# Kernel optimization log

Measured on AMD Instinct MI355X. Metric: run time of the kernel, lower is better.

Reference implementation:

```python
import jax, jax.numpy as jnp
import numpy as np

N, IN_DIM, HID, STEPS = 1024, 16, 64, 3
EDGE_P = 0.02


def setup_inputs() -> dict:
    key = jax.random.key(0)
    ks = jax.random.split(key, 10)
    s = 0.1
    A = (jax.random.uniform(ks[0], (N, N)) < EDGE_P).astype(jnp.float32)
    E = jax.random.uniform(ks[1], (N, N), dtype=jnp.float32)
    X = jax.random.normal(ks[2], (N, IN_DIM), dtype=jnp.float32)
    W_enc = jax.random.normal(ks[3], (HID, IN_DIM), dtype=jnp.float32) * s
    b_enc = jnp.zeros((HID,), jnp.float32)
    W_msg = jax.random.normal(ks[4], (HID, HID + 1), dtype=jnp.float32) * s
    b_msg = jnp.zeros((HID,), jnp.float32)
    W_ih = jax.random.normal(ks[5], (3 * HID, HID), dtype=jnp.float32) * s
    W_hh = jax.random.normal(ks[6], (3 * HID, HID), dtype=jnp.float32) * s
    b_ih = jnp.zeros((3 * HID,), jnp.float32)
    b_hh = jnp.zeros((3 * HID,), jnp.float32)
    W_r1 = jax.random.normal(ks[7], (HID, 2 * HID), dtype=jnp.float32) * s
    b_r1 = jnp.zeros((HID,), jnp.float32)
    W_r2 = jax.random.normal(ks[8], (1, HID), dtype=jnp.float32) * s
    b_r2 = jnp.zeros((1,), jnp.float32)
    return dict(A=A, E=E, X=X, W_enc=W_enc, b_enc=b_enc, W_msg=W_msg, b_msg=b_msg,
                W_ih=W_ih, W_hh=W_hh, b_ih=b_ih, b_hh=b_hh,
                W_r1=W_r1, b_r1=b_r1, W_r2=W_r2, b_r2=b_r2,
                source=3, target=7, steps=STEPS)


def _gru_cell(x, h, W_ih, W_hh, b_ih, b_hh):
    # torch.nn.GRUCell semantics, gate order (r, z, n)
    gi = x @ W_ih.T + b_ih
    gh = h @ W_hh.T + b_hh
    ir, iz, inn = jnp.split(gi, 3, axis=-1)
    hr, hz, hn = jnp.split(gh, 3, axis=-1)
    r = jax.nn.sigmoid(ir + hr)
    z = jax.nn.sigmoid(iz + hz)
    nct = jnp.tanh(inn + r * hn)
    return (1.0 - z) * nct + z * h


def reference(A, E, X, W_enc, b_enc, W_msg, b_msg, W_ih, W_hh, b_ih, b_hh,
              W_r1, b_r1, W_r2, b_r2, source, target, steps):
    mask = (A > 0).astype(X.dtype)            # [n, n] neighbor mask (row u -> cols v)
    deg = mask.sum(axis=1, keepdims=True)     # [n, 1]
    Wm_h, w_e = W_msg[:, :-1], W_msg[:, -1]   # split msg Linear: hidden part + edge-scalar column
    h = jnp.tanh(X @ W_enc.T + b_enc)         # [n, hid]

    def step(h, _):
        proj = h @ Wm_h.T + b_msg                              # [n, hid] per-neighbor part
        m = jnp.tanh(proj[None, :, :] + E[:, :, None] * w_e)   # [n, n, hid] message u<-v
        s = jnp.einsum('uv,uvh->uh', mask, m)                  # masked sum over neighbors
        msgs = jnp.where(deg > 0, s / jnp.maximum(deg, 1.0), 0.0)  # mean; zero if no neighbors
        return _gru_cell(msgs, h, W_ih, W_hh, b_ih, b_hh), None

    h, _ = jax.lax.scan(step, h, None, length=steps)
    cat = jnp.concatenate([h[source], h[target]])              # [2*hid]
    hid = jax.nn.relu(cat @ W_r1.T + b_r1)
    out = hid @ W_r2.T + b_r2                                  # [1]
    return jax.nn.sigmoid(out)
```

## Files before the change

kernel.cpp:

```cpp
#include <hip/hip_runtime.h>
#include <math.h>

#define N 1024
#define IN_DIM 16
#define HID 64
#define MAXD 64

__device__ __forceinline__ float sigmoidf_(float x) {
    return 1.0f / (1.0f + __expf(-x));
}
__device__ __forceinline__ float ftanh_(float x) {
    float e = __expf(2.0f * x);
    return 1.0f - 2.0f / (e + 1.0f);
}
__device__ __forceinline__ unsigned rne16_(float f) {
    unsigned u = __float_as_uint(f);
    return (u + 0x7FFFu + ((u >> 16) & 1u)) >> 16;
}
__device__ __forceinline__ float blo_(unsigned u) {
    return __uint_as_float(u << 16);
}
__device__ __forceinline__ float bhi_(unsigned u) {
    return __uint_as_float(u & 0xFFFF0000u);
}

#define WIH_W 6144
#define WHH_W 6144
#define WMSG_W 2048
#define WPACK_W (WIH_W + WHH_W + WMSG_W)

__global__ void init_kernel(const float* __restrict__ X,
                            const float* __restrict__ W_enc,
                            const float* __restrict__ b_enc,
                            const float* __restrict__ W_msg,
                            const float* __restrict__ b_msg,
                            const float* __restrict__ W_ih,
                            const float* __restrict__ W_hh,
                            const float* __restrict__ W_r1,
                            const float* __restrict__ A,
                            const float* __restrict__ E,
                            float* __restrict__ h,
                            float* __restrict__ proj,
                            int* __restrict__ nbr,
                            float* __restrict__ ev,
                            float* __restrict__ deg,
                            unsigned* __restrict__ Wpack,
                            float* __restrict__ Wr1T) {
    int bid = blockIdx.x;
    int tid = threadIdx.x;
    int wave = tid >> 6;
    int lane = tid & 63;

    if (bid < 256) {
        int u = bid * 4 + wave;
        __shared__ float sh[4][HID];
        float acc = b_enc[lane];
#pragma unroll
        for (int k = 0; k < IN_DIM; ++k)
            acc += X[u * IN_DIM + k] * W_enc[lane * IN_DIM + k];
        float hv = tanhf(acc);
        h[u * HID + lane] = hv;
        sh[wave][lane] = hv;
        __syncthreads();
        float pacc = b_msg[lane];
        const float4* h4 = (const float4*)sh[wave];
#pragma unroll
        for (int k4 = 0; k4 < HID / 4; ++k4) {
            float4 hh = h4[k4];
            const float* w = &W_msg[lane * (HID + 1) + k4 * 4];
            pacc += hh.x * w[0] + hh.y * w[1] + hh.z * w[2] + hh.w * w[3];
        }
        proj[u * HID + lane] = pacc;
    } else if (bid < 1280) {
        int u = bid - 256;
        __shared__ unsigned long long balls[16];
        __shared__ int base[16];
        float evr[4];
        bool has[4];
#pragma unroll
        for (int ci = 0; ci < 4; ++ci) {
            int chunk = wave * 4 + ci;
            int v = chunk * 64 + lane;
            float a = A[u * N + v];
            bool hs = (a > 0.0f);
            has[ci] = hs;
            evr[ci] = E[u * N + v];
            unsigned long long b = __ballot(hs);
            if (lane == 0) balls[chunk] = b;
        }
        __syncthreads();
        if (tid == 0) {
            int s = 0;
#pragma unroll
            for (int c = 0; c < 16; ++c) {
                base[c] = s;
                s += __popcll(balls[c]);
            }
            deg[u] = (float)s;
        }
        __syncthreads();
#pragma unroll
        for (int ci = 0; ci < 4; ++ci) {
            int chunk = wave * 4 + ci;
            if (has[ci]) {
                unsigned long long b = balls[chunk];
                int slot = base[chunk] + __popcll(b & ((1ull << lane) - 1ull));
                if (slot < MAXD) {
                    nbr[u * MAXD + slot] = chunk * 64 + lane;
                    ev[u * MAXD + slot] = evr[ci];
                }
            }
        }
    } else {
        int t = (bid - 1280) * 256 + tid;
        if (t < WIH_W) {
            int k2 = t / 192, row = t % 192;
            int k = 2 * k2;
            unsigned lo = rne16_(W_ih[row * 64 + k]);
            unsigned hi = rne16_(W_ih[row * 64 + k + 1]);
            Wpack[t] = lo | (hi << 16);
        } else if (t < WIH_W + WHH_W) {
            int t0 = t - WIH_W;
            int k2 = t0 / 192, row = t0 % 192;
            int k = 2 * k2;
            unsigned lo = rne16_(W_hh[row * 64 + k]);
            unsigned hi = rne16_(W_hh[row * 64 + k + 1]);
            Wpack[t] = lo | (hi << 16);
        } else if (t < WPACK_W) {
            int t0 = t - WIH_W - WHH_W;
            int k2 = t0 >> 6, j = t0 & 63;
            int k = 2 * k2;
            unsigned lo = rne16_(W_msg[j * (HID + 1) + k]);
            unsigned hi = rne16_(W_msg[j * (HID + 1) + k + 1]);
            Wpack[t] = lo | (hi << 16);
        } else if (t < WPACK_W + 8192) {
            int t0 = t - WPACK_W;
            int j = t0 >> 7, k = t0 & 127;
            Wr1T[k * 64 + j] = W_r1[t0];
        }
    }
}

__global__ void step_kernel(const float* __restrict__ proj,
                            const float* __restrict__ W_msg,
                            const float* __restrict__ b_msg,
                            const float* __restrict__ hin,
                            const int* __restrict__ nbr,
                            const float* __restrict__ ev,
                            const float* __restrict__ deg,
                            const unsigned* __restrict__ Wpack,
                            const float* __restrict__ b_ih,
                            const float* __restrict__ b_hh,
                            float* __restrict__ hout,
                            float* __restrict__ projout,
                            int do_proj) {
    int tid = threadIdx.x;
    int wave = tid >> 6;
    int lane = tid & 63;
    int u = blockIdx.x * 4 + wave;

    __shared__ unsigned sw[WPACK_W];
    __shared__ float sm[4][2][HID];

    {
        const uint4* gsrc = (const uint4*)Wpack;
        uint4* dst = (uint4*)sw;
#pragma unroll
        for (int c = 0; c < WPACK_W / 4 / 256; ++c)
            dst[c * 256 + tid] = gsrc[c * 256 + tid];
    }

    float we = W_msg[lane * (HID + 1) + HID];
    float d = deg[u];
    int dn = (int)d;
    float hu = hin[u * HID + lane];
    float sum = 0.0f;
    int i = 0;
    for (; i + 8 <= dn; i += 8) {
        int4 na = *(const int4*)&nbr[u * MAXD + i];
        int4 nb = *(const int4*)&nbr[u * MAXD + i + 4];
        float4 ea = *(const float4*)&ev[u * MAXD + i];
        float4 eb = *(const float4*)&ev[u * MAXD + i + 4];
        float q0 = proj[na.x * HID + lane];
        float q1 = proj[na.y * HID + lane];
        float q2 = proj[na.z * HID + lane];
        float q3 = proj[na.w * HID + lane];
        float q4 = proj[nb.x * HID + lane];
        float q5 = proj[nb.y * HID + lane];
        float q6 = proj[nb.z * HID + lane];
        float q7 = proj[nb.w * HID + lane];
        sum += ftanh_(q0 + ea.x * we) + ftanh_(q1 + ea.y * we)
             + ftanh_(q2 + ea.z * we) + ftanh_(q3 + ea.w * we);
        sum += ftanh_(q4 + eb.x * we) + ftanh_(q5 + eb.y * we)
             + ftanh_(q6 + eb.z * we) + ftanh_(q7 + eb.w * we);
    }
    for (; i + 4 <= dn; i += 4) {
        int4 nb = *(const int4*)&nbr[u * MAXD + i];
        float4 e4 = *(const float4*)&ev[u * MAXD + i];
        float q0 = proj[nb.x * HID + lane];
        float q1 = proj[nb.y * HID + lane];
        float q2 = proj[nb.z * HID + lane];
        float q3 = proj[nb.w * HID + lane];
        sum += ftanh_(q0 + e4.x * we) + ftanh_(q1 + e4.y * we)
             + ftanh_(q2 + e4.z * we) + ftanh_(q3 + e4.w * we);
    }
    for (; i < dn; ++i)
        sum += ftanh_(proj[nbr[u * MAXD + i] * HID + lane]
                      + ev[u * MAXD + i] * we);
    float msg = (dn > 0) ? (sum / d) : 0.0f;

    sm[wave][0][lane] = msg;
    sm[wave][1][lane] = hu;
    __syncthreads();

    const unsigned* swih = sw;
    const unsigned* swhh = sw + WIH_W;
    float accR  = b_ih[lane]       + b_hh[lane];
    float accZ  = b_ih[64 + lane]  + b_hh[64 + lane];
    float accNi = b_ih[128 + lane];
    float accNh = b_hh[128 + lane];
    const float2* m2 = (const float2*)sm[wave][0];
    const float2* h2 = (const float2*)sm[wave][1];
#pragma unroll
    for (int k2 = 0; k2 < 32; ++k2) {
        float2 mv = m2[k2];
        float2 hv = h2[k2];
        unsigned wiR = swih[k2 * 192 + lane];
        unsigned wiZ = swih[k2 * 192 + 64 + lane];
        unsigned wiN = swih[k2 * 192 + 128 + lane];
        unsigned whR = swhh[k2 * 192 + lane];
        unsigned whZ = swhh[k2 * 192 + 64 + lane];
        unsigned whN = swhh[k2 * 192 + 128 + lane];
        accR  += mv.x * blo_(wiR) + mv.y * bhi_(wiR)
               + hv.x * blo_(whR) + hv.y * bhi_(whR);
        accZ  += mv.x * blo_(wiZ) + mv.y * bhi_(wiZ)
               + hv.x * blo_(whZ) + hv.y * bhi_(whZ);
        accNi += mv.x * blo_(wiN) + mv.y * bhi_(wiN);
        accNh += hv.x * blo_(whN) + hv.y * bhi_(whN);
    }
    float r = sigmoidf_(accR);
    float z = sigmoidf_(accZ);
    float n = ftanh_(accNi + r * accNh);
    float hnew = (1.0f - z) * n + z * hu;
    hout[u * HID + lane] = hnew;

    if (do_proj) {
        __syncthreads();
        sm[wave][0][lane] = hnew;
        __syncthreads();
        const unsigned* swmsg = sw + WIH_W + WHH_W;
        float pacc = b_msg[lane];
        const float2* n2 = (const float2*)sm[wave][0];
#pragma unroll
        for (int k2 = 0; k2 < 32; ++k2) {
            float2 hh = n2[k2];
            unsigned wm = swmsg[k2 * 64 + lane];
            pacc += hh.x * blo_(wm) + hh.y * bhi_(wm);
        }
        projout[u * HID + lane] = pacc;
    }
}

__global__ void readout_kernel(const float* __restrict__ h,
                               const float* __restrict__ Wr1T,
                               const float* __restrict__ b_r1,
                               const float* __restrict__ W_r2,
                               const float* __restrict__ b_r2,
                               const int* __restrict__ src,
                               const int* __restrict__ tgt,
                               float* __restrict__ out) {
    int lane = threadIdx.x;
    int sI = src[0];
    int tI = tgt[0];
    float acc = b_r1[lane];
#pragma unroll 8
    for (int k = 0; k < HID; ++k)
        acc += h[sI * HID + k] * Wr1T[k * 64 + lane];
#pragma unroll 8
    for (int k = 0; k < HID; ++k)
        acc += h[tI * HID + k] * Wr1T[(HID + k) * 64 + lane];
    float hid = fmaxf(acc, 0.0f);
    float p = hid * W_r2[lane];
#pragma unroll
    for (int off = 32; off > 0; off >>= 1)
        p += __shfl_down(p, off);
    if (lane == 0) out[0] = sigmoidf_(p + b_r2[0]);
}

extern "C" void kernel_launch(void* const* d_in, const int* in_sizes, int n_in,
                              void* d_out, int out_size, void* d_ws, size_t ws_size,
                              hipStream_t stream) {
    const float* A     = (const float*)d_in[0];
    const float* E     = (const float*)d_in[1];
    const float* X     = (const float*)d_in[2];
    const float* W_enc = (const float*)d_in[3];
    const float* b_enc = (const float*)d_in[4];
    const float* W_msg = (const float*)d_in[5];
    const float* b_msg = (const float*)d_in[6];
    const float* W_ih  = (const float*)d_in[7];
    const float* W_hh  = (const float*)d_in[8];
    const float* b_ih  = (const float*)d_in[9];
    const float* b_hh  = (const float*)d_in[10];
    const float* W_r1  = (const float*)d_in[11];
    const float* b_r1  = (const float*)d_in[12];
    const float* W_r2  = (const float*)d_in[13];
    const float* b_r2  = (const float*)d_in[14];
    const int*   src   = (const int*)d_in[15];
    const int*   tgt   = (const int*)d_in[16];

    float* ws    = (float*)d_ws;
    float* h0    = ws;
    float* h1    = h0 + N * HID;
    float* p0    = h1 + N * HID;
    float* p1    = p0 + N * HID;
    float* deg   = p1 + N * HID;
    float* ev    = deg + N;
    int*   nbr   = (int*)(ev + N * MAXD);
    unsigned* Wpack = (unsigned*)(nbr + N * MAXD);
    float* Wr1T  = (float*)(Wpack + WPACK_W);

    init_kernel<<<1368, 256, 0, stream>>>(X, W_enc, b_enc, W_msg, b_msg,
                                          W_ih, W_hh, W_r1, A, E,
                                          h0, p0, nbr, ev, deg, Wpack, Wr1T);

    float* hc = h0; float* hn = h1;
    float* pc = p0; float* pn = p1;
    for (int s = 0; s < 3; ++s) {
        step_kernel<<<N / 4, 256, 0, stream>>>(pc, W_msg, b_msg, hc, nbr, ev, deg,
                                               Wpack, b_ih, b_hh,
                                               hn, pn, (s < 2) ? 1 : 0);
        float* t = hc; hc = hn; hn = t;
        t = pc; pc = pn; pn = t;
    }

    readout_kernel<<<1, 64, 0, stream>>>(hc, Wr1T, b_r1, W_r2, b_r2, src, tgt,
                                         (float*)d_out);
}
```

Measured before the change: 41.86 us.

## Compute final GNN step only for source and target nodes fused with readout

The last message-passing step is replaced by a single-block kernel that runs aggregation and the GRU update only for the source and target nodes, then applies the readout MLP in the same block. This removes a full 256-block step launch plus the separate readout launch. The readout only needs those two rows and the final step depends on earlier states only, so the result is unchanged. The single block also reloads the packed GRU weights into shared memory, which adds a little latency on the critical path.

```diff
diff --git a/kernel.cpp b/kernel.cpp
--- a/kernel.cpp
+++ b/kernel.cpp
@@ -152,8 +152,7 @@
                             const float* __restrict__ b_ih,
                             const float* __restrict__ b_hh,
                             float* __restrict__ hout,
-                            float* __restrict__ projout,
-                            int do_proj) {
+                            float* __restrict__ projout) {
     int tid = threadIdx.x;
     int wave = tid >> 6;
     int lane = tid & 63;
@@ -244,47 +243,129 @@
     float hnew = (1.0f - z) * n + z * hu;
     hout[u * HID + lane] = hnew;
 
-    if (do_proj) {
-        __syncthreads();
-        sm[wave][0][lane] = hnew;
-        __syncthreads();
-        const unsigned* swmsg = sw + WIH_W + WHH_W;
-        float pacc = b_msg[lane];
-        const float2* n2 = (const float2*)sm[wave][0];
+    __syncthreads();
+    sm[wave][0][lane] = hnew;
+    __syncthreads();
+    const unsigned* swmsg = sw + WIH_W + WHH_W;
+    float pacc = b_msg[lane];
+    const float2* n2 = (const float2*)sm[wave][0];
+#pragma unroll
+    for (int k2 = 0; k2 < 32; ++k2) {
+        float2 hh = n2[k2];
+        unsigned wm = swmsg[k2 * 64 + lane];
+        pacc += hh.x * blo_(wm) + hh.y * bhi_(wm);
+    }
+    projout[u * HID + lane] = pacc;
+}
+
+__global__ void final_kernel(const float* __restrict__ proj,
+                             const float* __restrict__ W_msg,
+                             const float* __restrict__ hin,
+                             const int* __restrict__ nbr,
+                             const float* __restrict__ ev,
+                             const float* __restrict__ deg,
+                             const unsigned* __restrict__ Wpack,
+                             const float* __restrict__ b_ih,
+                             const float* __restrict__ b_hh,
+                             const float* __restrict__ Wr1T,
+                             const float* __restrict__ b_r1,
+                             const float* __restrict__ W_r2,
+                             const float* __restrict__ b_r2,
+                             const int* __restrict__ src,
+                             const int* __restrict__ tgt,
+                             float* __restrict__ out) {
+    int tid = threadIdx.x;
+    int wave = tid >> 6;
+    int lane = tid & 63;
+
+    __shared__ unsigned sw[WIH_W + WHH_W];
+    __shared__ float smh[2][HID];
+    __shared__ float smm[2][2][HID];
+
+    {
+        const uint4* gsrc = (const uint4*)Wpack;
+        uint4* dst = (uint4*)sw;
+#pragma unroll
+        for (int c = 0; c < (WIH_W + WHH_W) / 4 / 256; ++c)
+            dst[c * 256 + tid] = gsrc[c * 256 + tid];
+    }
+
+    float hu = 0.0f;
+    if (wave < 2) {
+        int u = (wave == 0) ? src[0] : tgt[0];
+        float we = W_msg[lane * (HID + 1) + HID];
+        float d = deg[u];
+        int dn = (int)d;
+        hu = hin[u * HID + lane];
+        float sum = 0.0f;
+        int i = 0;
+        for (; i + 4 <= dn; i += 4) {
+            int4 nb = *(const int4*)&nbr[u * MAXD + i];
+            float4 e4 = *(const float4*)&ev[u * MAXD + i];
+            float q0 = proj[nb.x * HID + lane];
+            float q1 = proj[nb.y * HID + lane];
+            float q2 = proj[nb.z * HID + lane];
+            float q3 = proj[nb.w * HID + lane];
+            sum += ftanh_(q0 + e4.x * we) + ftanh_(q1 + e4.y * we)
+                 + ftanh_(q2 + e4.z * we) + ftanh_(q3 + e4.w * we);
+        }
+        for (; i < dn; ++i)
+            sum += ftanh_(proj[nbr[u * MAXD + i] * HID + lane]
+                          + ev[u * MAXD + i] * we);
+        float msg = (dn > 0) ? (sum / d) : 0.0f;
+        smm[wave][0][lane] = msg;
+        smm[wave][1][lane] = hu;
+    }
+    __syncthreads();
+
+    if (wave < 2) {
+        const unsigned* swih = sw;
+        const unsigned* swhh = sw + WIH_W;
+        float accR  = b_ih[lane]       + b_hh[lane];
+        float accZ  = b_ih[64 + lane]  + b_hh[64 + lane];
+        float accNi = b_ih[128 + lane];
+        float accNh = b_hh[128 + lane];
+        const float2* m2 = (const float2*)smm[wave][0];
+        const float2* h2 = (const float2*)smm[wave][1];
 #pragma unroll
         for (int k2 = 0; k2 < 32; ++k2) {
-            float2 hh = n2[k2];
-            unsigned wm = swmsg[k2 * 64 + lane];
-            pacc += hh.x * blo_(wm) + hh.y * bhi_(wm);
-        }
-        projout[u * HID + lane] = pacc;
-    }
-}
-
-__global__ void readout_kernel(const float* __restrict__ h,
-                               const float* __restrict__ Wr1T,
-                               const float* __restrict__ b_r1,
-                               const float* __restrict__ W_r2,
-                               const float* __restrict__ b_r2,
-                               const int* __restrict__ src,
-                               const int* __restrict__ tgt,
-                               float* __restrict__ out) {
-    int lane = threadIdx.x;
-    int sI = src[0];
-    int tI = tgt[0];
-    float acc = b_r1[lane];
+            float2 mv = m2[k2];
+            float2 hv = h2[k2];
+            unsigned wiR = swih[k2 * 192 + lane];
+            unsigned wiZ = swih[k2 * 192 + 64 + lane];
+            unsigned wiN = swih[k2 * 192 + 128 + lane];
+            unsigned whR = swhh[k2 * 192 + lane];
+            unsigned whZ = swhh[k2 * 192 + 64 + lane];
+            unsigned whN = swhh[k2 * 192 + 128 + lane];
+            accR  += mv.x * blo_(wiR) + mv.y * bhi_(wiR)
+                   + hv.x * blo_(whR) + hv.y * bhi_(whR);
+            accZ  += mv.x * blo_(wiZ) + mv.y * bhi_(wiZ)
+                   + hv.x * blo_(whZ) + hv.y * bhi_(whZ);
+            accNi += mv.x * blo_(wiN) + mv.y * bhi_(wiN);
+            accNh += hv.x * blo_(whN) + hv.y * bhi_(whN);
+        }
+        float r = sigmoidf_(accR);
+        float z = sigmoidf_(accZ);
+        float n = ftanh_(accNi + r * accNh);
+        smh[wave][lane] = (1.0f - z) * n + z * hu;
+    }
+    __syncthreads();
+
+    if (wave == 0) {
+        float acc = b_r1[lane];
 #pragma unroll 8
-    for (int k = 0; k < HID; ++k)
-        acc += h[sI * HID + k] * Wr1T[k * 64 + lane];
+        for (int k = 0; k < HID; ++k)
+            acc += smh[0][k] * Wr1T[k * 64 + lane];
 #pragma unroll 8
-    for (int k = 0; k < HID; ++k)
-        acc += h[tI * HID + k] * Wr1T[(HID + k) * 64 + lane];
-    float hid = fmaxf(acc, 0.0f);
-    float p = hid * W_r2[lane];
-#pragma unroll
-    for (int off = 32; off > 0; off >>= 1)
-        p += __shfl_down(p, off);
-    if (lane == 0) out[0] = sigmoidf_(p + b_r2[0]);
+        for (int k = 0; k < HID; ++k)
+            acc += smh[1][k] * Wr1T[(HID + k) * 64 + lane];
+        float hid = fmaxf(acc, 0.0f);
+        float p = hid * W_r2[lane];
+#pragma unroll
+        for (int off = 32; off > 0; off >>= 1)
+            p += __shfl_down(p, off);
+        if (lane == 0) out[0] = sigmoidf_(p + b_r2[0]);
+    }
 }
 
 extern "C" void kernel_launch(void* const* d_in, const int* in_sizes, int n_in,
@@ -323,16 +404,13 @@
                                           W_ih, W_hh, W_r1, A, E,
                                           h0, p0, nbr, ev, deg, Wpack, Wr1T);
 
-    float* hc = h0; float* hn = h1;
-    float* pc = p0; float* pn = p1;
-    for (int s = 0; s < 3; ++s) {
-        step_kernel<<<N / 4, 256, 0, stream>>>(pc, W_msg, b_msg, hc, nbr, ev, deg,
-                                               Wpack, b_ih, b_hh,
-                                               hn, pn, (s < 2) ? 1 : 0);
-        float* t = hc; hc = hn; hn = t;
-        t = pc; pc = pn; pn = t;
-    }
-
-    readout_kernel<<<1, 64, 0, stream>>>(hc, Wr1T, b_r1, W_r2, b_r2, src, tgt,
-                                         (float*)d_out);
-}
+    step_kernel<<<N / 4, 256, 0, stream>>>(p0, W_msg, b_msg, h0, nbr, ev, deg,
+                                           Wpack, b_ih, b_hh, h1, p1);
+    step_kernel<<<N / 4, 256, 0, stream>>>(p1, W_msg, b_msg, h1, nbr, ev, deg,
+                                           Wpack, b_ih, b_hh, h0, p0);
+
+    final_kernel<<<1, 256, 0, stream>>>(p0, W_msg, h0, nbr, ev, deg,
+                                        Wpack, b_ih, b_hh,
+                                        Wr1T, b_r1, W_r2, b_r2, src, tgt,
+                                        (float*)d_out);
+}
```

Result: no change. 41.94 us (+0.2%).

## Compute only source/target nodes in final step and fuse readout via last-block ticket

Applied to the files above, without the earlier changes.

Drops the full third GNN step and the separate readout launch. The second step kernel now uses an atomic ticket so the last finishing block recomputes the final GRU update only for the source and target nodes, then runs the readout MLP in the same block. This removes one full N-node step and one kernel launch. In exchange it relies on threadfence and atomic ordering across blocks, and the tail work is serialised in a single block.

```diff
diff --git a/kernel.cpp b/kernel.cpp
--- a/kernel.cpp
+++ b/kernel.cpp
@@ -5,6 +5,7 @@
 #define IN_DIM 16
 #define HID 64
 #define MAXD 64
+#define SBLK 256
 
 __device__ __forceinline__ float sigmoidf_(float x) {
     return 1.0f / (1.0f + __expf(-x));
@@ -17,12 +18,8 @@
     unsigned u = __float_as_uint(f);
     return (u + 0x7FFFu + ((u >> 16) & 1u)) >> 16;
 }
-__device__ __forceinline__ float blo_(unsigned u) {
-    return __uint_as_float(u << 16);
-}
-__device__ __forceinline__ float bhi_(unsigned u) {
-    return __uint_as_float(u & 0xFFFF0000u);
-}
+__device__ __forceinline__ float blo_(unsigned u) { return __uint_as_float(u << 16); }
+__device__ __forceinline__ float bhi_(unsigned u) { return __uint_as_float(u & 0xFFFF0000u); }
 
 #define WIH_W 6144
 #define WHH_W 6144
@@ -45,7 +42,8 @@
                             float* __restrict__ ev,
                             float* __restrict__ deg,
                             unsigned* __restrict__ Wpack,
-                            float* __restrict__ Wr1T) {
+                            float* __restrict__ Wr1T,
+                            unsigned* __restrict__ ticket) {
     int bid = blockIdx.x;
     int tid = threadIdx.x;
     int wave = tid >> 6;
@@ -138,6 +136,7 @@
             int j = t0 >> 7, k = t0 & 127;
             Wr1T[k * 64 + j] = W_r1[t0];
         }
+        if (bid == 1280 && tid == 0) ticket[0] = 0u;
     }
 }
 
@@ -153,7 +152,15 @@
                             const float* __restrict__ b_hh,
                             float* __restrict__ hout,
                             float* __restrict__ projout,
-                            int do_proj) {
+                            int finalize,
+                            unsigned* __restrict__ ticket,
+                            const float* __restrict__ Wr1T,
+                            const float* __restrict__ b_r1,
+                            const float* __restrict__ W_r2,
+                            const float* __restrict__ b_r2,
+                            const int* __restrict__ src,
+                            const int* __restrict__ tgt,
+                            float* __restrict__ out) {
     int tid = threadIdx.x;
     int wave = tid >> 6;
     int lane = tid & 63;
@@ -161,6 +168,8 @@
 
     __shared__ unsigned sw[WPACK_W];
     __shared__ float sm[4][2][HID];
+    __shared__ float h3s[2][HID];
+    __shared__ int sfin;
 
     {
         const uint4* gsrc = (const uint4*)Wpack;
@@ -244,47 +253,99 @@
     float hnew = (1.0f - z) * n + z * hu;
     hout[u * HID + lane] = hnew;
 
-    if (do_proj) {
-        __syncthreads();
-        sm[wave][0][lane] = hnew;
-        __syncthreads();
-        const unsigned* swmsg = sw + WIH_W + WHH_W;
-        float pacc = b_msg[lane];
-        const float2* n2 = (const float2*)sm[wave][0];
+    __syncthreads();
+    sm[wave][0][lane] = hnew;
+    __syncthreads();
+    const unsigned* swmsg = sw + WIH_W + WHH_W;
+    float pacc = b_msg[lane];
+    const float2* n2 = (const float2*)sm[wave][0];
+#pragma unroll
+    for (int k2 = 0; k2 < 32; ++k2) {
+        float2 hh = n2[k2];
+        unsigned wm = swmsg[k2 * 64 + lane];
+        pacc += hh.x * blo_(wm) + hh.y * bhi_(wm);
+    }
+    projout[u * HID + lane] = pacc;
+
+    if (!finalize) return;
+    __threadfence();
+    __syncthreads();
+    if (tid == 0) {
+        unsigned t = atomicAdd(ticket, 1u);
+        sfin = (t == SBLK - 1) ? 1 : 0;
+    }
+    __syncthreads();
+    if (!sfin) return;
+    __threadfence();
+
+    if (wave < 2) {
+        int uu = (wave == 0) ? src[0] : tgt[0];
+        float dd = deg[uu];
+        int dn2 = min((int)dd, MAXD);
+        float sum2 = 0.0f;
+        int j = 0;
+        for (; j + 4 <= dn2; j += 4) {
+            int4 nb = *(const int4*)&nbr[uu * MAXD + j];
+            float4 e4 = *(const float4*)&ev[uu * MAXD + j];
+            float q0 = projout[nb.x * HID + lane];
+            float q1 = projout[nb.y * HID + lane];
+            float q2 = projout[nb.z * HID + lane];
+            float q3 = projout[nb.w * HID + lane];
+            sum2 += ftanh_(q0 + e4.x * we) + ftanh_(q1 + e4.y * we)
+                  + ftanh_(q2 + e4.z * we) + ftanh_(q3 + e4.w * we);
+        }
+        for (; j < dn2; ++j)
+            sum2 += ftanh_(projout[nbr[uu * MAXD + j] * HID + lane]
+                           + ev[uu * MAXD + j] * we);
+        float msg2 = (dn2 > 0) ? (sum2 / dd) : 0.0f;
+        float hu2 = hout[uu * HID + lane];
+        sm[wave][0][lane] = msg2;
+        sm[wave][1][lane] = hu2;
+        float aR  = b_ih[lane]       + b_hh[lane];
+        float aZ  = b_ih[64 + lane]  + b_hh[64 + lane];
+        float aNi = b_ih[128 + lane];
+        float aNh = b_hh[128 + lane];
+        const float2* mm2 = (const float2*)sm[wave][0];
+        const float2* hh2 = (const float2*)sm[wave][1];
 #pragma unroll
         for (int k2 = 0; k2 < 32; ++k2) {
-            float2 hh = n2[k2];
-            unsigned wm = swmsg[k2 * 64 + lane];
-            pacc += hh.x * blo_(wm) + hh.y * bhi_(wm);
-        }
-        projout[u * HID + lane] = pacc;
-    }
-}
-
-__global__ void readout_kernel(const float* __restrict__ h,
-                               const float* __restrict__ Wr1T,
-                               const float* __restrict__ b_r1,
-                               const float* __restrict__ W_r2,
-                               const float* __restrict__ b_r2,
-                               const int* __restrict__ src,
-                               const int* __restrict__ tgt,
-                               float* __restrict__ out) {
-    int lane = threadIdx.x;
-    int sI = src[0];
-    int tI = tgt[0];
-    float acc = b_r1[lane];
+            float2 mv = mm2[k2];
+            float2 hv = hh2[k2];
+            unsigned wiR = swih[k2 * 192 + lane];
+            unsigned wiZ = swih[k2 * 192 + 64 + lane];
+            unsigned wiN = swih[k2 * 192 + 128 + lane];
+            unsigned whR = swhh[k2 * 192 + lane];
+            unsigned whZ = swhh[k2 * 192 + 64 + lane];
+            unsigned whN = swhh[k2 * 192 + 128 + lane];
+            aR  += mv.x * blo_(wiR) + mv.y * bhi_(wiR)
+                 + hv.x * blo_(whR) + hv.y * bhi_(whR);
+            aZ  += mv.x * blo_(wiZ) + mv.y * bhi_(wiZ)
+                 + hv.x * blo_(whZ) + hv.y * bhi_(whZ);
+            aNi += mv.x * blo_(wiN) + mv.y * bhi_(wiN);
+            aNh += hv.x * blo_(whN) + hv.y * bhi_(whN);
+        }
+        float r2 = sigmoidf_(aR);
+        float z2 = sigmoidf_(aZ);
+        float n2r = ftanh_(aNi + r2 * aNh);
+        h3s[wave][lane] = (1.0f - z2) * n2r + z2 * hu2;
+    }
+    __syncthreads();
+
+    if (wave == 0) {
+        float acc = b_r1[lane];
 #pragma unroll 8
-    for (int k = 0; k < HID; ++k)
-        acc += h[sI * HID + k] * Wr1T[k * 64 + lane];
+        for (int k = 0; k < HID; ++k)
+            acc += h3s[0][k] * Wr1T[k * 64 + lane];
 #pragma unroll 8
-    for (int k = 0; k < HID; ++k)
-        acc += h[tI * HID + k] * Wr1T[(HID + k) * 64 + lane];
-    float hid = fmaxf(acc, 0.0f);
-    float p = hid * W_r2[lane];
-#pragma unroll
-    for (int off = 32; off > 0; off >>= 1)
-        p += __shfl_down(p, off);
-    if (lane == 0) out[0] = sigmoidf_(p + b_r2[0]);
+        for (int k = 0; k < HID; ++k)
+            acc += h3s[1][k] * Wr1T[(HID + k) * 64 + lane];
+        float hid = fmaxf(acc, 0.0f);
+        float p = hid * W_r2[lane];
+#pragma unroll
+        for (int off = 32; off > 0; off >>= 1)
+            p += __shfl_down(p, off);
+        if (lane == 0) out[0] = sigmoidf_(p + b_r2[0]);
+    }
 }
 
 extern "C" void kernel_launch(void* const* d_in, const int* in_sizes, int n_in,
@@ -318,21 +379,19 @@
     int*   nbr   = (int*)(ev + N * MAXD);
     unsigned* Wpack = (unsigned*)(nbr + N * MAXD);
     float* Wr1T  = (float*)(Wpack + WPACK_W);
+    unsigned* ticket = (unsigned*)(Wr1T + 128 * 64);
 
     init_kernel<<<1368, 256, 0, stream>>>(X, W_enc, b_enc, W_msg, b_msg,
                                           W_ih, W_hh, W_r1, A, E,
-                                          h0, p0, nbr, ev, deg, Wpack, Wr1T);
-
-    float* hc = h0; float* hn = h1;
-    float* pc = p0; float* pn = p1;
-    for (int s = 0; s < 3; ++s) {
-        step_kernel<<<N / 4, 256, 0, stream>>>(pc, W_msg, b_msg, hc, nbr, ev, deg,
-                                               Wpack, b_ih, b_hh,
-                                               hn, pn, (s < 2) ? 1 : 0);
-        float* t = hc; hc = hn; hn = t;
-        t = pc; pc = pn; pn = t;
-    }
-
-    readout_kernel<<<1, 64, 0, stream>>>(hc, Wr1T, b_r1, W_r2, b_r2, src, tgt,
-                                         (float*)d_out);
-}
+                                          h0, p0, nbr, ev, deg, Wpack, Wr1T,
+                                          ticket);
+
+    step_kernel<<<SBLK, 256, 0, stream>>>(p0, W_msg, b_msg, h0, nbr, ev, deg,
+                                          Wpack, b_ih, b_hh, h1, p1,
+                                          0, ticket, Wr1T, b_r1, W_r2, b_r2,
+                                          src, tgt, (float*)d_out);
+    step_kernel<<<SBLK, 256, 0, stream>>>(p1, W_msg, b_msg, h1, nbr, ev, deg,
+                                          Wpack, b_ih, b_hh, h0, p0,
+                                          1, ticket, Wr1T, b_r1, W_r2, b_r2,
+                                          src, tgt, (float*)d_out);
+}
```

After: 61.43 us. +46.7%, slower.
